# Kernel optimization log

Measured on AMD Instinct MI355X. Metric: run time of the kernel, lower is better.

Reference implementation:

```python
import jax, jax.numpy as jnp
import numpy as np

NUM_NODES = 50000
NUM_EDGES = 50000  # hyperedges
NNZ = 500000       # incidence entries
D_IN = 256
D_OUT = 256


def setup_inputs() -> dict:
    key = jax.random.key(0)
    k1, k2, k3, k4, k5, k6 = jax.random.split(key, 6)
    x = jax.random.normal(k1, (NUM_NODES, D_IN), dtype=jnp.float32)
    node_idx = jax.random.randint(k2, (NNZ,), 0, NUM_NODES, dtype=jnp.int64)
    edge_idx = jax.random.randint(k3, (NNZ,), 0, NUM_EDGES, dtype=jnp.int64)
    hyperedge_index = jnp.stack([node_idx, edge_idx], axis=0)
    hyperedge_weight = jax.random.uniform(k4, (NUM_EDGES,), dtype=jnp.float32)
    # PyG Linear(in, heads*out, bias=False) weight, stored here as [in, out]
    W = jax.random.normal(k5, (D_IN, D_OUT), dtype=jnp.float32) / np.sqrt(D_IN)
    b = jax.random.normal(k6, (D_OUT,), dtype=jnp.float32) * 0.01
    return {"x": x, "hyperedge_index": hyperedge_index,
            "hyperedge_weight": hyperedge_weight, "W": W, "b": b}


def reference(x, hyperedge_index, hyperedge_weight, W, b):
    # PyG HypergraphConv, use_attention=False, heads=1, concat=True:
    #   X' = D^{-1} H B^{-1} H^T (X Theta) + bias, with W folded into D.
    num_nodes = x.shape[0]
    num_edges = hyperedge_weight.shape[0]
    node_idx = hyperedge_index[0]
    edge_idx = hyperedge_index[1]

    xl = x @ W  # [N, F] linear transform (no bias in lin)

    # D[i] = sum over incident hyperedges of their weight; invert, inf -> 0
    D = jax.ops.segment_sum(hyperedge_weight[edge_idx], node_idx,
                            num_segments=num_nodes)
    Dinv = jnp.where(D > 0, 1.0 / D, 0.0)

    # B[e] = hyperedge cardinality; invert, inf -> 0
    Bc = jax.ops.segment_sum(jnp.ones((node_idx.shape[0],), dtype=xl.dtype),
                             edge_idx, num_segments=num_edges)
    Binv = jnp.where(Bc > 0, 1.0 / Bc, 0.0)

    # node -> hyperedge: message = B^{-1}[e] * xl[i], summed per hyperedge
    e_feat = jax.ops.segment_sum(Binv[edge_idx][:, None] * xl[node_idx],
                                 edge_idx, num_segments=num_edges)  # [E, F]

    # hyperedge -> node: message = D^{-1}[i] * e_feat[e], summed per node
    out = jax.ops.segment_sum(Dinv[node_idx][:, None] * e_feat[edge_idx],
                              node_idx, num_segments=num_nodes)  # [N, F]

    return out + b
```

## Files before the change

### kernel.cpp

```cpp
#include <hip/hip_runtime.h>
#include <hip/hip_bf16.h>

#define NUM_NODES 50000
#define NUM_EDGES 50000
#define NNZ       500000
#define D_IN      256
#define D_OUT     256
#define HB        128
#define HWORDS    25000
#define CHUNK     3907

typedef __attribute__((ext_vector_type(8))) short  bf16x8;
typedef __attribute__((ext_vector_type(4))) float  f32x4;

static __device__ __forceinline__ float bf2f(unsigned short u) {
    return __uint_as_float(((unsigned)u) << 16);
}
static __device__ __forceinline__ unsigned short f2bf(float f) {
    unsigned u = __float_as_uint(f);
    u += 0x7FFFu + ((u >> 16) & 1u);
    return (unsigned short)(u >> 16);
}

__global__ __launch_bounds__(256) void hist_kernel(
    const int* __restrict__ node_idx, const int* __restrict__ edge_idx,
    unsigned int* __restrict__ HbE, unsigned int* __restrict__ HbN)
{
    const int arr = blockIdx.y;
    const int* __restrict__ idx = arr ? node_idx : edge_idx;
    unsigned int* __restrict__ Hb = arr ? HbN : HbE;
    __shared__ unsigned int h[HWORDS];
    for (int wdi = threadIdx.x; wdi < HWORDS; wdi += 256) h[wdi] = 0;
    __syncthreads();
    int beg = blockIdx.x * CHUNK;
    int end = min(NNZ, beg + CHUNK);
    for (int i = beg + (int)threadIdx.x; i < end; i += 256) {
        int k = idx[i];
        atomicAdd(&h[k >> 1], 1u << ((k & 1) * 16));
    }
    __syncthreads();
    unsigned int* out = Hb + (size_t)blockIdx.x * HWORDS;
    for (int wdi = threadIdx.x; wdi < HWORDS; wdi += 256) out[wdi] = h[wdi];
}

__global__ __launch_bounds__(256) void hreduce_kernel(
    unsigned int* __restrict__ HbE, unsigned int* __restrict__ HbN,
    int* __restrict__ Bc, int* __restrict__ node_cnt)
{
    const int arr = blockIdx.y;
    unsigned int* __restrict__ Hb = arr ? HbN : HbE;
    int* __restrict__ cnt = arr ? node_cnt : Bc;
    int wdi = blockIdx.x * 256 + (int)threadIdx.x;
    if (wdi >= HWORDS) return;
    unsigned int s0 = 0, s1 = 0;
    for (int b = 0; b < HB; ++b) {
        unsigned int u = Hb[(size_t)b * HWORDS + wdi];
        Hb[(size_t)b * HWORDS + wdi] = (s0 & 0xffffu) | (s1 << 16);
        s0 += u & 0xffffu;
        s1 += u >> 16;
    }
    cnt[2 * wdi]     = (int)s0;
    cnt[2 * wdi + 1] = (int)s1;
}

__global__ __launch_bounds__(256) void scan1_kernel(
    const int* __restrict__ cntE, const int* __restrict__ cntN,
    int* __restrict__ offE, int* __restrict__ offN, int* __restrict__ bsums)
{
    const int arr = blockIdx.y;
    const int* cnt = arr ? cntN : cntE;
    int* off       = arr ? offN : offE;
    int tid = threadIdx.x;
    int i = blockIdx.x * 256 + tid;
    int v = (i < 50000) ? cnt[i] : 0;
    __shared__ int sh[256];
    sh[tid] = v;
    __syncthreads();
    for (int s = 1; s < 256; s <<= 1) {
        int t = (tid >= s) ? sh[tid - s] : 0;
        __syncthreads();
        sh[tid] += t;
        __syncthreads();
    }
    if (i < 50000) off[i] = sh[tid] - v;
    if (tid == 255) bsums[arr * 196 + blockIdx.x] = sh[255];
}

__global__ __launch_bounds__(256) void scan2_kernel(
    const int* __restrict__ bsums, int* __restrict__ bsum_off)
{
    __shared__ int sh[256];
    int tid = threadIdx.x;
    for (int arr = 0; arr < 2; ++arr) {
        int v = (tid < 196) ? bsums[arr * 196 + tid] : 0;
        sh[tid] = v;
        __syncthreads();
        for (int s = 1; s < 256; s <<= 1) {
            int t = (tid >= s) ? sh[tid - s] : 0;
            __syncthreads();
            sh[tid] += t;
            __syncthreads();
        }
        if (tid < 196) bsum_off[arr * 196 + tid] = sh[tid] - v;
        __syncthreads();
    }
}

__global__ __launch_bounds__(256) void scan3_kernel(
    const int* __restrict__ bsum_off, int* __restrict__ offE, int* __restrict__ offN)
{
    const int arr = blockIdx.y;
    int* off = arr ? offN : offE;
    int i = blockIdx.x * 256 + threadIdx.x;
    if (i < 50000) off[i] += bsum_off[arr * 196 + blockIdx.x];
    if (blockIdx.x == 0 && threadIdx.x == 0) off[50000] = NNZ;
}

__global__ __launch_bounds__(256) void fill_kernel(
    const int* __restrict__ node_idx, const int* __restrict__ edge_idx,
    const unsigned int* __restrict__ HbE, const unsigned int* __restrict__ HbN,
    const int* __restrict__ edge_off, const int* __restrict__ node_off,
    int* __restrict__ edge_nodes, int* __restrict__ node_edges)
{
    const int arr = blockIdx.y;
    const int* __restrict__ key = arr ? node_idx : edge_idx;
    const int* __restrict__ val = arr ? edge_idx : node_idx;
    const unsigned int* __restrict__ Hb = arr ? HbN : HbE;
    const int* __restrict__ off = arr ? node_off : edge_off;
    int* __restrict__ out       = arr ? node_edges : edge_nodes;

    __shared__ unsigned int h[HWORDS];
    const unsigned int* hrow = Hb + (size_t)blockIdx.x * HWORDS;
    for (int wdi = threadIdx.x; wdi < HWORDS; wdi += 256) h[wdi] = hrow[wdi];
    __syncthreads();

    int beg = blockIdx.x * CHUNK;
    int end = min(NNZ, beg + CHUNK);
    for (int i = beg + (int)threadIdx.x; i < end; i += 256) {
        int k = key[i];
        int sh = (k & 1) * 16;
        unsigned int old = atomicAdd(&h[k >> 1], 1u << sh);
        int rank = (int)((old >> sh) & 0xffffu);
        out[off[k] + rank] = val[i];
    }
}

__global__ __launch_bounds__(256) void transpose_w_kernel(
    const float* __restrict__ W, unsigned short* __restrict__ Wt)
{
    int n = blockIdx.x, k = threadIdx.x;
    Wt[n * 256 + k] = f2bf(W[k * 256 + n]);
}

__global__ __launch_bounds__(256) void gemm_kernel(
    const float* __restrict__ x, const unsigned short* __restrict__ Wt,
    unsigned short* __restrict__ xl)
{
    __shared__ __align__(16) unsigned short sA[64 * 32];
    __shared__ __align__(16) unsigned short sB[256 * 32];

    const int tid  = threadIdx.x;
    const int l    = tid & 63;
    const int wq   = tid >> 6;
    const int quad = l >> 4;
    const int l15  = l & 15;
    const int m0   = blockIdx.x * 64;

    f32x4 acc[4][4];
    #pragma unroll
    for (int i = 0; i < 4; ++i)
        #pragma unroll
        for (int j = 0; j < 4; ++j) acc[i][j] = (f32x4){0.f, 0.f, 0.f, 0.f};

    const int ar = tid >> 2, ag = tid & 3;
    int agm = m0 + ar; if (agm > NUM_NODES - 1) agm = NUM_NODES - 1;
    const float* aptr = x + (size_t)agm * D_IN + ag * 8;
    unsigned short* aout = &sA[ar * 32 + (ag ^ ((ar >> 1) & 3)) * 8];

    for (int k0 = 0; k0 < D_IN; k0 += 32) {
        {
            float4 v0 = *(const float4*)(aptr + k0);
            float4 v1 = *(const float4*)(aptr + k0 + 4);
            bf16x8 av;
            av[0] = (short)f2bf(v0.x); av[1] = (short)f2bf(v0.y);
            av[2] = (short)f2bf(v0.z); av[3] = (short)f2bf(v0.w);
            av[4] = (short)f2bf(v1.x); av[5] = (short)f2bf(v1.y);
            av[6] = (short)f2bf(v1.z); av[7] = (short)f2bf(v1.w);
            *(bf16x8*)aout = av;
        }
        #pragma unroll
        for (int i = 0; i < 4; ++i) {
            int c = i * 256 + tid;
            int row = c >> 2, g = c & 3;
            bf16x8 bv = *(const bf16x8*)(Wt + row * 256 + k0 + g * 8);
            int s = g ^ ((row >> 1) & 3);
            *(bf16x8*)(&sB[row * 32 + s * 8]) = bv;
        }
        __syncthreads();

        bf16x8 af[4], bfr[4];
        #pragma unroll
        for (int mi = 0; mi < 4; ++mi) {
            int r = mi * 16 + l15;
            int s = quad ^ ((r >> 1) & 3);
            af[mi] = *(const bf16x8*)(&sA[r * 32 + s * 8]);
        }
        #pragma unroll
        for (int ni = 0; ni < 4; ++ni) {
            int r = wq * 64 + ni * 16 + l15;
            int s = quad ^ ((r >> 1) & 3);
            bfr[ni] = *(const bf16x8*)(&sB[r * 32 + s * 8]);
        }
        #pragma unroll
        for (int mi = 0; mi < 4; ++mi)
            #pragma unroll
            for (int ni = 0; ni < 4; ++ni)
                acc[mi][ni] = __builtin_amdgcn_mfma_f32_16x16x32_bf16(
                    af[mi], bfr[ni], acc[mi][ni], 0, 0, 0);
        __syncthreads();
    }

    #pragma unroll
    for (int mi = 0; mi < 4; ++mi) {
        #pragma unroll
        for (int ni = 0; ni < 4; ++ni) {
            int col = wq * 64 + ni * 16 + l15;
            #pragma unroll
            for (int r = 0; r < 4; ++r) {
                int m = m0 + mi * 16 + quad * 4 + r;
                if (m < NUM_NODES)
                    xl[(size_t)m * D_OUT + col] = f2bf(acc[mi][ni][r]);
            }
        }
    }
}

__global__ __launch_bounds__(256) void edge_agg_kernel(
    const unsigned short* __restrict__ xl,
    const int* __restrict__ edge_off, const int* __restrict__ edge_nodes,
    unsigned short* __restrict__ e_feat)
{
    int e = blockIdx.x * 4 + (threadIdx.x >> 6);
    int lane = threadIdx.x & 63;
    if (e >= NUM_EDGES) return;
    int beg = edge_off[e], end = edge_off[e + 1];
    float ax = 0.f, ay = 0.f, az = 0.f, aw = 0.f;
    int j = beg;
    for (; j + 4 <= end; j += 4) {
        int n0 = edge_nodes[j];
        int n1 = edge_nodes[j + 1];
        int n2 = edge_nodes[j + 2];
        int n3 = edge_nodes[j + 3];
        ushort4 u0 = *(const ushort4*)(xl + (size_t)n0 * D_OUT + lane * 4);
        ushort4 u1 = *(const ushort4*)(xl + (size_t)n1 * D_OUT + lane * 4);
        ushort4 u2 = *(const ushort4*)(xl + (size_t)n2 * D_OUT + lane * 4);
        ushort4 u3 = *(const ushort4*)(xl + (size_t)n3 * D_OUT + lane * 4);
        ax += bf2f(u0.x) + bf2f(u1.x) + bf2f(u2.x) + bf2f(u3.x);
        ay += bf2f(u0.y) + bf2f(u1.y) + bf2f(u2.y) + bf2f(u3.y);
        az += bf2f(u0.z) + bf2f(u1.z) + bf2f(u2.z) + bf2f(u3.z);
        aw += bf2f(u0.w) + bf2f(u1.w) + bf2f(u2.w) + bf2f(u3.w);
    }
    for (; j < end; ++j) {
        int node = edge_nodes[j];
        ushort4 u = *(const ushort4*)(xl + (size_t)node * D_OUT + lane * 4);
        ax += bf2f(u.x); ay += bf2f(u.y); az += bf2f(u.z); aw += bf2f(u.w);
    }
    float binv = (end > beg) ? 1.0f / (float)(end - beg) : 0.0f;
    ushort4 o;
    o.x = f2bf(ax * binv); o.y = f2bf(ay * binv);
    o.z = f2bf(az * binv); o.w = f2bf(aw * binv);
    *(ushort4*)(e_feat + (size_t)e * D_OUT + lane * 4) = o;
}

__global__ __launch_bounds__(256) void node_agg_kernel(
    const unsigned short* __restrict__ e_feat,
    const int* __restrict__ node_off, const int* __restrict__ node_edges,
    const float* __restrict__ w, const float* __restrict__ bias,
    float* __restrict__ out)
{
    int n = blockIdx.x * 4 + (threadIdx.x >> 6);
    int lane = threadIdx.x & 63;
    if (n >= NUM_NODES) return;
    int beg = node_off[n], end = node_off[n + 1];
    float ax = 0.f, ay = 0.f, az = 0.f, aw = 0.f;
    float dsum = 0.f;
    int j = beg;
    for (; j + 4 <= end; j += 4) {
        int e0 = node_edges[j];
        int e1 = node_edges[j + 1];
        int e2 = node_edges[j + 2];
        int e3 = node_edges[j + 3];
        ushort4 u0 = *(const ushort4*)(e_feat + (size_t)e0 * D_OUT + lane * 4);
        ushort4 u1 = *(const ushort4*)(e_feat + (size_t)e1 * D_OUT + lane * 4);
        ushort4 u2 = *(const ushort4*)(e_feat + (size_t)e2 * D_OUT + lane * 4);
        ushort4 u3 = *(const ushort4*)(e_feat + (size_t)e3 * D_OUT + lane * 4);
        dsum += w[e0] + w[e1] + w[e2] + w[e3];
        ax += bf2f(u0.x) + bf2f(u1.x) + bf2f(u2.x) + bf2f(u3.x);
        ay += bf2f(u0.y) + bf2f(u1.y) + bf2f(u2.y) + bf2f(u3.y);
        az += bf2f(u0.z) + bf2f(u1.z) + bf2f(u2.z) + bf2f(u3.z);
        aw += bf2f(u0.w) + bf2f(u1.w) + bf2f(u2.w) + bf2f(u3.w);
    }
    for (; j < end; ++j) {
        int e = node_edges[j];
        dsum += w[e];
        ushort4 u = *(const ushort4*)(e_feat + (size_t)e * D_OUT + lane * 4);
        ax += bf2f(u.x); ay += bf2f(u.y); az += bf2f(u.z); aw += bf2f(u.w);
    }
    float dinv = (dsum > 0.0f) ? 1.0f / dsum : 0.0f;
    float4 bv = *(const float4*)(bias + lane * 4);
    float4 o;
    o.x = ax * dinv + bv.x;
    o.y = ay * dinv + bv.y;
    o.z = az * dinv + bv.z;
    o.w = aw * dinv + bv.w;
    *(float4*)(out + (size_t)n * D_OUT + lane * 4) = o;
}

extern "C" void kernel_launch(void* const* d_in, const int* in_sizes, int n_in,
                              void* d_out, int out_size, void* d_ws, size_t ws_size,
                              hipStream_t stream) {
    const float* x    = (const float*)d_in[0];
    const int*   hidx = (const int*)d_in[1];
    const float* w    = (const float*)d_in[2];
    const float* W    = (const float*)d_in[3];
    const float* b    = (const float*)d_in[4];
    const int* node_idx = hidx;
    const int* edge_idx = hidx + NNZ;

    char* ws = (char*)d_ws;
    size_t off = 0;
    auto alloc = [&](size_t bytes) -> void* {
        off = (off + 511) & ~(size_t)511;
        void* p = ws + off;
        off += bytes;
        return p;
    };
    unsigned short* xl     = (unsigned short*)alloc((size_t)NUM_NODES * D_OUT * 2);
    unsigned short* e_feat = (unsigned short*)alloc((size_t)NUM_EDGES * D_OUT * 2);
    int* Bc         = (int*)alloc(50000 * sizeof(int));
    int* node_cnt   = (int*)alloc(50000 * sizeof(int));
    int* edge_off   = (int*)alloc((NUM_EDGES + 1) * sizeof(int));
    int* node_off   = (int*)alloc((NUM_NODES + 1) * sizeof(int));
    int* edge_nodes = (int*)alloc((size_t)NNZ * sizeof(int));
    int* node_edges = (int*)alloc((size_t)NNZ * sizeof(int));
    unsigned short* Wt = (unsigned short*)alloc(256 * 256 * 2);
    int* bsums    = (int*)alloc(392 * sizeof(int));
    int* bsum_off = (int*)alloc(392 * sizeof(int));

    unsigned int* HbE = (unsigned int*)xl;
    unsigned int* HbN = (unsigned int*)e_feat;

    hist_kernel<<<dim3(HB, 2), 256, 0, stream>>>(node_idx, edge_idx, HbE, HbN);
    hreduce_kernel<<<dim3((HWORDS + 255) / 256, 2), 256, 0, stream>>>(HbE, HbN, Bc, node_cnt);
    scan1_kernel<<<dim3(196, 2), 256, 0, stream>>>(Bc, node_cnt, edge_off, node_off, bsums);
    scan2_kernel<<<1, 256, 0, stream>>>(bsums, bsum_off);
    scan3_kernel<<<dim3(196, 2), 256, 0, stream>>>(bsum_off, edge_off, node_off);
    fill_kernel<<<dim3(HB, 2), 256, 0, stream>>>(node_idx, edge_idx, HbE, HbN,
                                                 edge_off, node_off, edge_nodes, node_edges);
    transpose_w_kernel<<<256, 256, 0, stream>>>(W, Wt);
    gemm_kernel<<<(NUM_NODES + 63) / 64, 256, 0, stream>>>(x, Wt, xl);
    edge_agg_kernel<<<NUM_EDGES / 4, 256, 0, stream>>>(xl, edge_off, edge_nodes, e_feat);
    node_agg_kernel<<<NUM_NODES / 4, 256, 0, stream>>>(e_feat, node_off, node_edges, w, b,
                                                       (float*)d_out);
}
```

Measured before the change: 254.7 us.

## Fuse CSR build into one cooperative kernel and make GEMM persistent with resident W

Merges histogram, per-block prefix, scan stages, W transpose and CSR fill into a single cooperative kernel separated by grid syncs. The final offset fix-up is folded into the consumers, which add the per-chunk block sums when reading offsets. The GEMM becomes persistent over 256 blocks, keeps all of bf16 W in LDS (128KB) and processes 32-row tiles. The aim is to remove many kernel launches and repeated W reloads. In exchange it adds grid-sync costs and very large LDS use, which limits the GEMM to one block per CU with less latency hiding.

```diff
diff --git a/kernel.cpp b/kernel.cpp
--- a/kernel.cpp
+++ b/kernel.cpp
@@ -1,5 +1,8 @@
 #include <hip/hip_runtime.h>
 #include <hip/hip_bf16.h>
+#include <hip/hip_cooperative_groups.h>
+
+namespace cg = cooperative_groups;
 
 #define NUM_NODES 50000
 #define NUM_EDGES 50000
@@ -9,6 +12,8 @@
 #define HB        128
 #define HWORDS    25000
 #define CHUNK     3907
+#define NBLK      196
+#define GEMM_TILES 1563
 
 typedef __attribute__((ext_vector_type(8))) short  bf16x8;
 typedef __attribute__((ext_vector_type(4))) float  f32x4;
@@ -22,214 +27,205 @@
     return (unsigned short)(u >> 16);
 }
 
-__global__ __launch_bounds__(256) void hist_kernel(
+__global__ __launch_bounds__(256) void prep_kernel(
     const int* __restrict__ node_idx, const int* __restrict__ edge_idx,
-    unsigned int* __restrict__ HbE, unsigned int* __restrict__ HbN)
+    const float* __restrict__ W, unsigned short* __restrict__ Wt,
+    unsigned int* __restrict__ HbE, unsigned int* __restrict__ HbN,
+    int* __restrict__ Bc, int* __restrict__ node_cnt,
+    int* __restrict__ edge_off, int* __restrict__ node_off,
+    int* __restrict__ bsums, int* __restrict__ bsum_off,
+    int* __restrict__ edge_nodes, int* __restrict__ node_edges)
 {
-    const int arr = blockIdx.y;
+    cg::grid_group grid = cg::this_grid();
+    __shared__ unsigned int h[HWORDS];
+    __shared__ int sh[256];
+
+    const int tid = (int)threadIdx.x;
+    const int bid = (int)blockIdx.x;
+    const int arr = bid >> 7;
+    const int hb  = bid & 127;
+
+    Wt[bid * 256 + tid] = f2bf(W[(size_t)tid * 256 + bid]);
+
     const int* __restrict__ idx = arr ? node_idx : edge_idx;
     unsigned int* __restrict__ Hb = arr ? HbN : HbE;
-    __shared__ unsigned int h[HWORDS];
-    for (int wdi = threadIdx.x; wdi < HWORDS; wdi += 256) h[wdi] = 0;
+    for (int i = tid; i < HWORDS; i += 256) h[i] = 0;
     __syncthreads();
-    int beg = blockIdx.x * CHUNK;
-    int end = min(NNZ, beg + CHUNK);
-    for (int i = beg + (int)threadIdx.x; i < end; i += 256) {
+    const int beg = hb * CHUNK;
+    const int end = min(NNZ, beg + CHUNK);
+    for (int i = beg + tid; i < end; i += 256) {
         int k = idx[i];
         atomicAdd(&h[k >> 1], 1u << ((k & 1) * 16));
     }
     __syncthreads();
-    unsigned int* out = Hb + (size_t)blockIdx.x * HWORDS;
-    for (int wdi = threadIdx.x; wdi < HWORDS; wdi += 256) out[wdi] = h[wdi];
-}
-
-__global__ __launch_bounds__(256) void hreduce_kernel(
-    unsigned int* __restrict__ HbE, unsigned int* __restrict__ HbN,
-    int* __restrict__ Bc, int* __restrict__ node_cnt)
-{
-    const int arr = blockIdx.y;
-    unsigned int* __restrict__ Hb = arr ? HbN : HbE;
-    int* __restrict__ cnt = arr ? node_cnt : Bc;
-    int wdi = blockIdx.x * 256 + (int)threadIdx.x;
-    if (wdi >= HWORDS) return;
-    unsigned int s0 = 0, s1 = 0;
-    for (int b = 0; b < HB; ++b) {
-        unsigned int u = Hb[(size_t)b * HWORDS + wdi];
-        Hb[(size_t)b * HWORDS + wdi] = (s0 & 0xffffu) | (s1 << 16);
-        s0 += u & 0xffffu;
-        s1 += u >> 16;
-    }
-    cnt[2 * wdi]     = (int)s0;
-    cnt[2 * wdi + 1] = (int)s1;
-}
-
-__global__ __launch_bounds__(256) void scan1_kernel(
-    const int* __restrict__ cntE, const int* __restrict__ cntN,
-    int* __restrict__ offE, int* __restrict__ offN, int* __restrict__ bsums)
-{
-    const int arr = blockIdx.y;
-    const int* cnt = arr ? cntN : cntE;
-    int* off       = arr ? offN : offE;
-    int tid = threadIdx.x;
-    int i = blockIdx.x * 256 + tid;
-    int v = (i < 50000) ? cnt[i] : 0;
-    __shared__ int sh[256];
-    sh[tid] = v;
-    __syncthreads();
-    for (int s = 1; s < 256; s <<= 1) {
-        int t = (tid >= s) ? sh[tid - s] : 0;
-        __syncthreads();
-        sh[tid] += t;
-        __syncthreads();
-    }
-    if (i < 50000) off[i] = sh[tid] - v;
-    if (tid == 255) bsums[arr * 196 + blockIdx.x] = sh[255];
-}
-
-__global__ __launch_bounds__(256) void scan2_kernel(
-    const int* __restrict__ bsums, int* __restrict__ bsum_off)
-{
-    __shared__ int sh[256];
-    int tid = threadIdx.x;
-    for (int arr = 0; arr < 2; ++arr) {
-        int v = (tid < 196) ? bsums[arr * 196 + tid] : 0;
+    {
+        unsigned int* o = Hb + (size_t)hb * HWORDS;
+        for (int i = tid; i < HWORDS; i += 256) o[i] = h[i];
+    }
+    grid.sync();
+
+    {
+        int wdi2 = bid * 196 + tid;
+        if (tid < 196 && wdi2 < 50000) {
+            int a2 = wdi2 / HWORDS, wd = wdi2 % HWORDS;
+            unsigned int* __restrict__ H = a2 ? HbN : HbE;
+            int* __restrict__ cnt = a2 ? node_cnt : Bc;
+            unsigned int s0 = 0, s1 = 0;
+            #pragma unroll 8
+            for (int b2 = 0; b2 < HB; ++b2) {
+                unsigned int u = H[(size_t)b2 * HWORDS + wd];
+                H[(size_t)b2 * HWORDS + wd] = (s0 & 0xffffu) | (s1 << 16);
+                s0 += u & 0xffffu;
+                s1 += u >> 16;
+            }
+            cnt[2 * wd]     = (int)s0;
+            cnt[2 * wd + 1] = (int)s1;
+        }
+    }
+    grid.sync();
+
+    for (int sc = bid; sc < 2 * NBLK; sc += 256) {
+        int a3 = sc / NBLK, ch = sc % NBLK;
+        const int* cnt = a3 ? node_cnt : Bc;
+        int* off       = a3 ? node_off : edge_off;
+        int i = ch * 256 + tid;
+        int v = (i < 50000) ? cnt[i] : 0;
         sh[tid] = v;
         __syncthreads();
         for (int s = 1; s < 256; s <<= 1) {
-            int t = (tid >= s) ? sh[tid - s] : 0;
+            int t2 = (tid >= s) ? sh[tid - s] : 0;
             __syncthreads();
-            sh[tid] += t;
+            sh[tid] += t2;
             __syncthreads();
         }
-        if (tid < 196) bsum_off[arr * 196 + tid] = sh[tid] - v;
-        __syncthreads();
-    }
-}
-
-__global__ __launch_bounds__(256) void scan3_kernel(
-    const int* __restrict__ bsum_off, int* __restrict__ offE, int* __restrict__ offN)
-{
-    const int arr = blockIdx.y;
-    int* off = arr ? offN : offE;
-    int i = blockIdx.x * 256 + threadIdx.x;
-    if (i < 50000) off[i] += bsum_off[arr * 196 + blockIdx.x];
-    if (blockIdx.x == 0 && threadIdx.x == 0) off[50000] = NNZ;
-}
-
-__global__ __launch_bounds__(256) void fill_kernel(
-    const int* __restrict__ node_idx, const int* __restrict__ edge_idx,
-    const unsigned int* __restrict__ HbE, const unsigned int* __restrict__ HbN,
-    const int* __restrict__ edge_off, const int* __restrict__ node_off,
-    int* __restrict__ edge_nodes, int* __restrict__ node_edges)
-{
-    const int arr = blockIdx.y;
-    const int* __restrict__ key = arr ? node_idx : edge_idx;
-    const int* __restrict__ val = arr ? edge_idx : node_idx;
-    const unsigned int* __restrict__ Hb = arr ? HbN : HbE;
-    const int* __restrict__ off = arr ? node_off : edge_off;
-    int* __restrict__ out       = arr ? node_edges : edge_nodes;
-
-    __shared__ unsigned int h[HWORDS];
-    const unsigned int* hrow = Hb + (size_t)blockIdx.x * HWORDS;
-    for (int wdi = threadIdx.x; wdi < HWORDS; wdi += 256) h[wdi] = hrow[wdi];
-    __syncthreads();
-
-    int beg = blockIdx.x * CHUNK;
-    int end = min(NNZ, beg + CHUNK);
-    for (int i = beg + (int)threadIdx.x; i < end; i += 256) {
-        int k = key[i];
-        int sh = (k & 1) * 16;
-        unsigned int old = atomicAdd(&h[k >> 1], 1u << sh);
-        int rank = (int)((old >> sh) & 0xffffu);
-        out[off[k] + rank] = val[i];
-    }
-}
-
-__global__ __launch_bounds__(256) void transpose_w_kernel(
-    const float* __restrict__ W, unsigned short* __restrict__ Wt)
-{
-    int n = blockIdx.x, k = threadIdx.x;
-    Wt[n * 256 + k] = f2bf(W[k * 256 + n]);
+        if (i < 50000) off[i] = sh[tid] - v;
+        if (tid == 255) bsums[a3 * NBLK + ch] = sh[255];
+        __syncthreads();
+    }
+    grid.sync();
+
+    if (bid == 0) {
+        for (int a4 = 0; a4 < 2; ++a4) {
+            int v = (tid < NBLK) ? bsums[a4 * NBLK + tid] : 0;
+            sh[tid] = v;
+            __syncthreads();
+            for (int s = 1; s < 256; s <<= 1) {
+                int t2 = (tid >= s) ? sh[tid - s] : 0;
+                __syncthreads();
+                sh[tid] += t2;
+                __syncthreads();
+            }
+            if (tid < NBLK) bsum_off[a4 * NBLK + tid] = sh[tid] - v;
+            if (tid == NBLK - 1) {
+                int* off = a4 ? node_off : edge_off;
+                off[50000] = NNZ - (sh[tid] - v);
+            }
+            __syncthreads();
+        }
+    }
+    grid.sync();
+
+    {
+        const unsigned int* hrow = Hb + (size_t)hb * HWORDS;
+        for (int i = tid; i < HWORDS; i += 256) h[i] = hrow[i];
+        const int* __restrict__ key = arr ? node_idx : edge_idx;
+        const int* __restrict__ val = arr ? edge_idx : node_idx;
+        const int* __restrict__ off = arr ? node_off : edge_off;
+        const int* __restrict__ bs  = bsum_off + arr * NBLK;
+        int* __restrict__ out       = arr ? node_edges : edge_nodes;
+        __syncthreads();
+        for (int i = beg + tid; i < end; i += 256) {
+            int k = key[i];
+            int shb = (k & 1) * 16;
+            unsigned int old = atomicAdd(&h[k >> 1], 1u << shb);
+            int rank = (int)((old >> shb) & 0xffffu);
+            out[off[k] + bs[k >> 8] + rank] = val[i];
+        }
+    }
 }
 
 __global__ __launch_bounds__(256) void gemm_kernel(
     const float* __restrict__ x, const unsigned short* __restrict__ Wt,
     unsigned short* __restrict__ xl)
 {
-    __shared__ __align__(16) unsigned short sA[64 * 32];
-    __shared__ __align__(16) unsigned short sB[256 * 32];
-
-    const int tid  = threadIdx.x;
+    __shared__ __align__(16) unsigned short sW[256 * 256];
+    __shared__ __align__(16) unsigned short sA[32 * 256];
+
+    const int tid  = (int)threadIdx.x;
     const int l    = tid & 63;
     const int wq   = tid >> 6;
     const int quad = l >> 4;
     const int l15  = l & 15;
-    const int m0   = blockIdx.x * 64;
-
-    f32x4 acc[4][4];
-    #pragma unroll
-    for (int i = 0; i < 4; ++i)
+
+    for (int i = tid; i < 8192; i += 256) {
+        int n = i >> 5, g = i & 31;
+        int gs = g ^ (n & 31);
+        *(bf16x8*)(&sW[n * 256 + gs * 8]) = *(const bf16x8*)(Wt + n * 256 + g * 8);
+    }
+
+    for (int tile = blockIdx.x; tile < GEMM_TILES; tile += 256) {
+        const int m0 = tile * 32;
+        __syncthreads();
+        {
+            int row = tid >> 3, p = tid & 7;
+            int gm = m0 + row; if (gm > NUM_NODES - 1) gm = NUM_NODES - 1;
+            const float* src = x + (size_t)gm * D_IN + p * 32;
+            #pragma unroll
+            for (int j = 0; j < 4; ++j) {
+                float4 v0 = *(const float4*)(src + j * 8);
+                float4 v1 = *(const float4*)(src + j * 8 + 4);
+                bf16x8 av;
+                av[0] = (short)f2bf(v0.x); av[1] = (short)f2bf(v0.y);
+                av[2] = (short)f2bf(v0.z); av[3] = (short)f2bf(v0.w);
+                av[4] = (short)f2bf(v1.x); av[5] = (short)f2bf(v1.y);
+                av[6] = (short)f2bf(v1.z); av[7] = (short)f2bf(v1.w);
+                int u  = p * 4 + j;
+                int us = u ^ (row & 7);
+                *(bf16x8*)(&sA[row * 256 + us * 8]) = av;
+            }
+        }
+        __syncthreads();
+
+        f32x4 acc[2][4];
         #pragma unroll
-        for (int j = 0; j < 4; ++j) acc[i][j] = (f32x4){0.f, 0.f, 0.f, 0.f};
-
-    const int ar = tid >> 2, ag = tid & 3;
-    int agm = m0 + ar; if (agm > NUM_NODES - 1) agm = NUM_NODES - 1;
-    const float* aptr = x + (size_t)agm * D_IN + ag * 8;
-    unsigned short* aout = &sA[ar * 32 + (ag ^ ((ar >> 1) & 3)) * 8];
-
-    for (int k0 = 0; k0 < D_IN; k0 += 32) {
-        {
-            float4 v0 = *(const float4*)(aptr + k0);
-            float4 v1 = *(const float4*)(aptr + k0 + 4);
-            bf16x8 av;
-            av[0] = (short)f2bf(v0.x); av[1] = (short)f2bf(v0.y);
-            av[2] = (short)f2bf(v0.z); av[3] = (short)f2bf(v0.w);
-            av[4] = (short)f2bf(v1.x); av[5] = (short)f2bf(v1.y);
-            av[6] = (short)f2bf(v1.z); av[7] = (short)f2bf(v1.w);
-            *(bf16x8*)aout = av;
-        }
+        for (int i = 0; i < 2; ++i)
+            #pragma unroll
+            for (int j = 0; j < 4; ++j) acc[i][j] = (f32x4){0.f, 0.f, 0.f, 0.f};
+
         #pragma unroll
-        for (int i = 0; i < 4; ++i) {
-            int c = i * 256 + tid;
-            int row = c >> 2, g = c & 3;
-            bf16x8 bv = *(const bf16x8*)(Wt + row * 256 + k0 + g * 8);
-            int s = g ^ ((row >> 1) & 3);
-            *(bf16x8*)(&sB[row * 32 + s * 8]) = bv;
-        }
-        __syncthreads();
-
-        bf16x8 af[4], bfr[4];
+        for (int k0 = 0; k0 < 8; ++k0) {
+            bf16x8 af[2], bfr[4];
+            #pragma unroll
+            for (int mi = 0; mi < 2; ++mi) {
+                int r  = mi * 16 + l15;
+                int us = (k0 * 4 + quad) ^ (r & 7);
+                af[mi] = *(const bf16x8*)(&sA[r * 256 + us * 8]);
+            }
+            #pragma unroll
+            for (int ni = 0; ni < 4; ++ni) {
+                int n  = wq * 64 + ni * 16 + l15;
+                int gs = (k0 * 4 + quad) ^ (n & 31);
+                bfr[ni] = *(const bf16x8*)(&sW[n * 256 + gs * 8]);
+            }
+            #pragma unroll
+            for (int mi = 0; mi < 2; ++mi)
+                #pragma unroll
+                for (int ni = 0; ni < 4; ++ni)
+                    acc[mi][ni] = __builtin_amdgcn_mfma_f32_16x16x32_bf16(
+                        af[mi], bfr[ni], acc[mi][ni], 0, 0, 0);
+        }
+
         #pragma unroll
-        for (int mi = 0; mi < 4; ++mi) {
-            int r = mi * 16 + l15;
-            int s = quad ^ ((r >> 1) & 3);
-            af[mi] = *(const bf16x8*)(&sA[r * 32 + s * 8]);
-        }
-        #pragma unroll
-        for (int ni = 0; ni < 4; ++ni) {
-            int r = wq * 64 + ni * 16 + l15;
-            int s = quad ^ ((r >> 1) & 3);
-            bfr[ni] = *(const bf16x8*)(&sB[r * 32 + s * 8]);
-        }
-        #pragma unroll
-        for (int mi = 0; mi < 4; ++mi)
-            #pragma unroll
-            for (int ni = 0; ni < 4; ++ni)
-                acc[mi][ni] = __builtin_amdgcn_mfma_f32_16x16x32_bf16(
-                    af[mi], bfr[ni], acc[mi][ni], 0, 0, 0);
-        __syncthreads();
-    }
-
-    #pragma unroll
-    for (int mi = 0; mi < 4; ++mi) {
-        #pragma unroll
-        for (int ni = 0; ni < 4; ++ni) {
-            int col = wq * 64 + ni * 16 + l15;
-            #pragma unroll
-            for (int r = 0; r < 4; ++r) {
-                int m = m0 + mi * 16 + quad * 4 + r;
-                if (m < NUM_NODES)
-                    xl[(size_t)m * D_OUT + col] = f2bf(acc[mi][ni][r]);
+        for (int mi = 0; mi < 2; ++mi) {
+            #pragma unroll
+            for (int ni = 0; ni < 4; ++ni) {
+                int col = wq * 64 + ni * 16 + l15;
+                #pragma unroll
+                for (int r = 0; r < 4; ++r) {
+                    int m = m0 + mi * 16 + quad * 4 + r;
+                    if (m < NUM_NODES)
+                        xl[(size_t)m * D_OUT + col] = f2bf(acc[mi][ni][r]);
+                }
             }
         }
     }
@@ -237,13 +233,15 @@
 
 __global__ __launch_bounds__(256) void edge_agg_kernel(
     const unsigned short* __restrict__ xl,
-    const int* __restrict__ edge_off, const int* __restrict__ edge_nodes,
+    const int* __restrict__ edge_off, const int* __restrict__ bsE,
+    const int* __restrict__ edge_nodes,
     unsigned short* __restrict__ e_feat)
 {
     int e = blockIdx.x * 4 + (threadIdx.x >> 6);
     int lane = threadIdx.x & 63;
     if (e >= NUM_EDGES) return;
-    int beg = edge_off[e], end = edge_off[e + 1];
+    int beg = edge_off[e]     + bsE[e >> 8];
+    int end = edge_off[e + 1] + bsE[(e + 1) >> 8];
     float ax = 0.f, ay = 0.f, az = 0.f, aw = 0.f;
     int j = beg;
     for (; j + 4 <= end; j += 4) {
@@ -274,14 +272,16 @@
 
 __global__ __launch_bounds__(256) void node_agg_kernel(
     const unsigned short* __restrict__ e_feat,
-    const int* __restrict__ node_off, const int* __restrict__ node_edges,
+    const int* __restrict__ node_off, const int* __restrict__ bsN,
+    const int* __restrict__ node_edges,
     const float* __restrict__ w, const float* __restrict__ bias,
     float* __restrict__ out)
 {
     int n = blockIdx.x * 4 + (threadIdx.x >> 6);
     int lane = threadIdx.x & 63;
     if (n >= NUM_NODES) return;
-    int beg = node_off[n], end = node_off[n + 1];
+    int beg = node_off[n]     + bsN[n >> 8];
+    int end = node_off[n + 1] + bsN[(n + 1) >> 8];
     float ax = 0.f, ay = 0.f, az = 0.f, aw = 0.f;
     float dsum = 0.f;
     int j = beg;
@@ -344,22 +344,25 @@
     int* edge_nodes = (int*)alloc((size_t)NNZ * sizeof(int));
     int* node_edges = (int*)alloc((size_t)NNZ * sizeof(int));
     unsigned short* Wt = (unsigned short*)alloc(256 * 256 * 2);
-    int* bsums    = (int*)alloc(392 * sizeof(int));
-    int* bsum_off = (int*)alloc(392 * sizeof(int));
+    int* bsums    = (int*)alloc(2 * NBLK * sizeof(int));
+    int* bsum_off = (int*)alloc(2 * NBLK * sizeof(int));
 
     unsigned int* HbE = (unsigned int*)xl;
     unsigned int* HbN = (unsigned int*)e_feat;
 
-    hist_kernel<<<dim3(HB, 2), 256, 0, stream>>>(node_idx, edge_idx, HbE, HbN);
-    hreduce_kernel<<<dim3((HWORDS + 255) / 256, 2), 256, 0, stream>>>(HbE, HbN, Bc, node_cnt);
-    scan1_kernel<<<dim3(196, 2), 256, 0, stream>>>(Bc, node_cnt, edge_off, node_off, bsums);
-    scan2_kernel<<<1, 256, 0, stream>>>(bsums, bsum_off);
-    scan3_kernel<<<dim3(196, 2), 256, 0, stream>>>(bsum_off, edge_off, node_off);
-    fill_kernel<<<dim3(HB, 2), 256, 0, stream>>>(node_idx, edge_idx, HbE, HbN,
-                                                 edge_off, node_off, edge_nodes, node_edges);
-    transpose_w_kernel<<<256, 256, 0, stream>>>(W, Wt);
-    gemm_kernel<<<(NUM_NODES + 63) / 64, 256, 0, stream>>>(x, Wt, xl);
-    edge_agg_kernel<<<NUM_EDGES / 4, 256, 0, stream>>>(xl, edge_off, edge_nodes, e_feat);
-    node_agg_kernel<<<NUM_NODES / 4, 256, 0, stream>>>(e_feat, node_off, node_edges, w, b,
-                                                       (float*)d_out);
-}
+    {
+        void* args[] = {
+            (void*)&node_idx, (void*)&edge_idx, (void*)&W, (void*)&Wt,
+            (void*)&HbE, (void*)&HbN, (void*)&Bc, (void*)&node_cnt,
+            (void*)&edge_off, (void*)&node_off, (void*)&bsums, (void*)&bsum_off,
+            (void*)&edge_nodes, (void*)&node_edges
+        };
+        hipLaunchCooperativeKernel((const void*)prep_kernel, dim3(256), dim3(256),
+                                   args, 0, stream);
+    }
+    gemm_kernel<<<256, 256, 0, stream>>>(x, Wt, xl);
+    edge_agg_kernel<<<NUM_EDGES / 4, 256, 0, stream>>>(xl, edge_off, bsum_off,
+                                                       edge_nodes, e_feat);
+    node_agg_kernel<<<NUM_NODES / 4, 256, 0, stream>>>(e_feat, node_off, bsum_off + NBLK,
+                                                       node_edges, w, b, (float*)d_out);
+}
```

Measured after the change: 384.9 us. +51.1%, slower.
